# Kernel tuning notes

Hardware: AMD Instinct MI355X
Metric: run time of the kernel (lower is better)

## Reference

```python
import jax, jax.numpy as jnp
import numpy as np

# Mamba2 config (matches mamba_ssm.Mamba2 defaults used by the wrapper)
D_MODEL = 1024
D_STATE = 128
D_CONV = 4
EXPAND = 2
HEADDIM = 64
CHUNK = 256
D_INNER = EXPAND * D_MODEL            # 2048
NHEADS = D_INNER // HEADDIM           # 32
CONV_DIM = D_INNER + 2 * D_STATE      # 2304 (x, B, C share the causal conv)
D_IN_PROJ = 2 * D_INNER + 2 * D_STATE + NHEADS  # z, xBC, dt
EPS = 1e-5


def rmsnorm(x, w, eps=EPS):
    return x * jax.lax.rsqrt(jnp.mean(x * x, axis=-1, keepdims=True) + eps) * w


def setup_inputs() -> dict:
    key = jax.random.key(0)
    ks = jax.random.split(key, 8)
    B, L = 2, 2048
    def w(k, shape, sc=0.02):
        return jax.random.normal(k, shape, jnp.float32) * sc
    return {
        "x": jax.random.normal(ks[0], (B, L, D_MODEL), jnp.float32),
        "norm_w": jnp.ones((D_MODEL,), jnp.float32),
        "in_proj_w": w(ks[1], (D_IN_PROJ, D_MODEL)),
        "conv_w": w(ks[2], (CONV_DIM, 1, D_CONV), 0.2),   # depthwise kernel
        "conv_b": jnp.zeros((CONV_DIM,), jnp.float32),
        "dt_bias": w(ks[3], (NHEADS,), 1.0),
        "A_log": jnp.log(1.0 + 15.0 * jax.random.uniform(ks[4], (NHEADS,), jnp.float32)),
        "D": jnp.ones((NHEADS,), jnp.float32),
        "gnorm_w": jnp.ones((D_INNER,), jnp.float32),
        "out_proj_w": w(ks[5], (D_MODEL, D_INNER)),
    }


def _ssd(xd, a, Bm, Cm):
    """Chunked SSD scan (ssd_minimal_discrete).
    xd: (b,l,h,p) = x*dt ; a: (b,l,h) = dt*A ; Bm,Cm: (b,l,n) (ngroups=1)."""
    b, l, h, p = xd.shape
    n = Bm.shape[-1]
    nc = l // CHUNK
    xd = xd.reshape(b, nc, CHUNK, h, p)
    a = a.reshape(b, nc, CHUNK, h).transpose(0, 3, 1, 2)   # (b,h,nc,c)
    Bm = Bm.reshape(b, nc, CHUNK, n)
    Cm = Cm.reshape(b, nc, CHUNK, n)
    a_cs = jnp.cumsum(a, axis=-1)                           # (b,h,nc,c)
    # 1) intra-chunk: causal decay matrix L[t,s] = exp(sum_{s<i<=t} a_i)
    diff = a_cs[..., :, None] - a_cs[..., None, :]          # (b,h,nc,c,c)
    mask = jnp.tril(jnp.ones((CHUNK, CHUNK), bool))
    Lm = jnp.exp(jnp.where(mask, diff, 0.0)) * mask
    Y_diag = jnp.einsum("bcln,bcsn,bhcls,bcshp->bclhp", Cm, Bm, Lm, xd)
    # 2) per-chunk end states
    decay_states = jnp.exp(a_cs[..., -1:] - a_cs)           # (b,h,nc,c)
    states = jnp.einsum("bcln,bhcl,bclhp->bchpn", Bm, decay_states, xd)
    # 3) inter-chunk recurrence (vectorized segsum over the 8+1 chunk totals)
    tot = jnp.pad(a_cs[..., -1], ((0, 0), (0, 0), (1, 0)))  # (b,h,nc+1)
    tot_cs = jnp.cumsum(tot, axis=-1)
    dchunk = tot_cs[..., :, None] - tot_cs[..., None, :]    # (b,h,nc+1,nc+1)
    cmask = jnp.tril(jnp.ones((nc + 1, nc + 1), bool))
    dchunk = jnp.exp(jnp.where(cmask, dchunk, 0.0)) * cmask
    states = jnp.concatenate([jnp.zeros_like(states[:, :1]), states], axis=1)
    new_states = jnp.einsum("bhzc,bchpn->bzhpn", dchunk, states)
    init_states = new_states[:, :-1]                        # state entering each chunk
    # 4) state -> output contribution
    Y_off = jnp.einsum("bcln,bchpn,bhcl->bclhp", Cm, init_states, jnp.exp(a_cs))
    return (Y_diag + Y_off).reshape(b, l, h, p)


def reference(x, norm_w, in_proj_w, conv_w, conv_b, dt_bias, A_log, D, gnorm_w, out_proj_w):
    res = x
    u = rmsnorm(x, norm_w)
    zxbcdt = u @ in_proj_w.T                                # (b,l,d_in_proj)
    z, xBC, dt = jnp.split(zxbcdt, [D_INNER, D_INNER + CONV_DIM], axis=-1)
    # causal depthwise conv1d over (x,B,C), then SiLU
    xBC_t = jnp.pad(xBC.transpose(0, 2, 1), ((0, 0), (0, 0), (D_CONV - 1, 0)))
    conv = jax.lax.conv_general_dilated(
        xBC_t, conv_w, (1,), "VALID",
        dimension_numbers=("NCH", "OIH", "NCH"), feature_group_count=CONV_DIM)
    xBC = jax.nn.silu(conv.transpose(0, 2, 1) + conv_b)
    xs, Bm, Cm = jnp.split(xBC, [D_INNER, D_INNER + D_STATE], axis=-1)
    dt = jax.nn.softplus(dt + dt_bias)                      # (b,l,h)
    A = -jnp.exp(A_log)                                     # (h,)
    xh = xs.reshape(xs.shape[0], xs.shape[1], NHEADS, HEADDIM)
    y = _ssd(xh * dt[..., None], dt * A, Bm, Cm)
    y = y + D[None, None, :, None] * xh                     # skip term
    y = y.reshape(xs.shape)
    y = rmsnorm(y * jax.nn.silu(z), gnorm_w)                # gated RMSNorm
    return res + y @ out_proj_w.T
```

## Files before the change

### kernel.cpp

```cpp
#include <hip/hip_runtime.h>
#include <hip/hip_bf16.h>

typedef __hip_bfloat16 bf16_t;
typedef __attribute__((ext_vector_type(8))) short bfrag8;
typedef __attribute__((ext_vector_type(4))) float floatx4;

#define DM     1024
#define DI     2048
#define NHD    32
#define HD     64
#define DSTATE 128
#define CONVD  2304
#define NPROJ  4384
#define NPAD   4480
#define MR     4096
#define LL     2048
#define EPSF   1e-5f
#define PSTR   40

__device__ __forceinline__ void gl_lds16(const void* g, void* l) {
  __builtin_amdgcn_global_load_lds((const __attribute__((address_space(1))) void*)g,
                                   (__attribute__((address_space(3))) void*)l, 16, 0, 0);
}
__device__ __forceinline__ unsigned pack_bf16_rn(float a, float b) {
  unsigned ua = (__float_as_uint(a) + 0x8000u) >> 16;
  unsigned ub = (__float_as_uint(b) + 0x8000u) >> 16;
  return ua | (ub << 16);
}
__device__ __forceinline__ unsigned short bf16u(float a) {
  return (unsigned short)((__float_as_uint(a) + 0x8000u) >> 16);
}
__device__ __forceinline__ float blo(unsigned u){ return __uint_as_float(u << 16); }
__device__ __forceinline__ float bhi(unsigned u){ return __uint_as_float(u & 0xffff0000u); }

__global__ void rms1_kernel(const float* __restrict__ x, const float* __restrict__ w,
                            bf16_t* __restrict__ ub) {
  int row = blockIdx.x, t = threadIdx.x;
  float4 v = ((const float4*)(x + (long)row * DM))[t];
  float ss = v.x*v.x + v.y*v.y + v.z*v.z + v.w*v.w;
#pragma unroll
  for (int off = 32; off > 0; off >>= 1) ss += __shfl_down(ss, off, 64);
  __shared__ float red[4];
  if ((t & 63) == 0) red[t >> 6] = ss;
  __syncthreads();
  float tot = red[0] + red[1] + red[2] + red[3];
  float rs = rsqrtf(tot * (1.f / DM) + EPSF);
  float4 wv = ((const float4*)w)[t];
  bf16_t* o = ub + (long)row * DM + t * 4;
  o[0] = __float2bfloat16(v.x * rs * wv.x);
  o[1] = __float2bfloat16(v.y * rs * wv.y);
  o[2] = __float2bfloat16(v.z * rs * wv.z);
  o[3] = __float2bfloat16(v.w * rs * wv.w);
}

__global__ void cvtw1_kernel(const float* __restrict__ w, bf16_t* __restrict__ o) {
  int i4 = blockIdx.x * 256 + threadIdx.x;
  int idx = i4 * 4;
  int row = idx >> 10;
  float4 v = make_float4(0.f, 0.f, 0.f, 0.f);
  if (row < NPROJ) v = *(const float4*)(w + idx);
  bf16_t* d = o + idx;
  d[0] = __float2bfloat16(v.x); d[1] = __float2bfloat16(v.y);
  d[2] = __float2bfloat16(v.z); d[3] = __float2bfloat16(v.w);
}
__global__ void cvtw2_kernel(const float* __restrict__ w, bf16_t* __restrict__ o) {
  int i4 = blockIdx.x * 256 + threadIdx.x;
  int idx = i4 * 4;
  float4 v = *(const float4*)(w + idx);
  bf16_t* d = o + idx;
  d[0] = __float2bfloat16(v.x); d[1] = __float2bfloat16(v.y);
  d[2] = __float2bfloat16(v.z); d[3] = __float2bfloat16(v.w);
}

template<int TN, bool DO_RES, bool OUT_BF16>
__global__ __launch_bounds__(256) void gemm64_kernel(const bf16_t* __restrict__ A,
    const bf16_t* __restrict__ Bw, const float* __restrict__ resid,
    void* __restrict__ Cout, int N, int K) {
  __shared__ bf16_t As[128 * 64];
  __shared__ bf16_t Bs[TN * 64];
  const int tid = threadIdx.x;
  const int lane = tid & 63;
  const int wv = tid >> 6;
  const int l15 = lane & 15;
  const int l4 = lane >> 4;
  constexpr int MF = (TN == 128) ? 4 : 2;
  const int wm = (TN == 128) ? ((wv >> 1) << 6) : (wv << 5);
  const int wn = (TN == 128) ? ((wv & 1) << 6) : 0;
  const int tm = blockIdx.x << 7;
  const int tn = blockIdx.y * TN;

  floatx4 acc[MF][4];
#pragma unroll
  for (int i = 0; i < MF; i++)
#pragma unroll
    for (int j = 0; j < 4; j++) acc[i][j] = (floatx4){0.f, 0.f, 0.f, 0.f};

  const int r = tid >> 3;
  const int c8 = tid & 7;
  const int scol = ((c8 ^ (r & 7)) << 3);
  const bf16_t* Ag = A + (long)(tm + r) * K + scol;
  const bf16_t* Bg = Bw + (long)(tn + r) * K + scol;
  const int swz = l15 & 7;

  for (int k0 = 0; k0 < K; k0 += 64) {
#pragma unroll
    for (int q = 0; q < 4; q++)
      gl_lds16(Ag + (long)(q * 32) * K + k0, &As[q * 2048 + tid * 8]);
#pragma unroll
    for (int q = 0; q < TN / 32; q++)
      gl_lds16(Bg + (long)(q * 32) * K + k0, &Bs[q * 2048 + tid * 8]);
    __syncthreads();
#pragma unroll
    for (int kk = 0; kk < 2; kk++) {
      bfrag8 af[MF], bfr[4];
      const int ch = ((kk << 2) | l4) ^ swz;
#pragma unroll
      for (int j = 0; j < 4; j++)
        bfr[j] = *(const bfrag8*)&Bs[(wn + j * 16 + l15) * 64 + ch * 8];
#pragma unroll
      for (int i = 0; i < MF; i++)
        af[i] = *(const bfrag8*)&As[(wm + i * 16 + l15) * 64 + ch * 8];
#pragma unroll
      for (int i = 0; i < MF; i++)
#pragma unroll
        for (int j = 0; j < 4; j++)
          acc[i][j] = __builtin_amdgcn_mfma_f32_16x16x32_bf16(af[i], bfr[j], acc[i][j], 0, 0, 0);
    }
    __syncthreads();
  }
#pragma unroll
  for (int i = 0; i < MF; i++)
#pragma unroll
    for (int j = 0; j < 4; j++)
#pragma unroll
      for (int r2 = 0; r2 < 4; r2++) {
        int row = tm + wm + i * 16 + l4 * 4 + r2;
        int col = tn + wn + j * 16 + l15;
        float v = acc[i][j][r2];
        if (OUT_BF16) {
          ((bf16_t*)Cout)[(long)row * N + col] = __float2bfloat16(v);
        } else {
          if (DO_RES) v += resid[(long)row * N + col];
          ((float*)Cout)[(long)row * N + col] = v;
        }
      }
}

__global__ __launch_bounds__(256) void gemm_s_kernel(const bf16_t* __restrict__ Cmh,
                const bf16_t* __restrict__ Bmh, float* __restrict__ SL) {
  __shared__ bf16_t As[128 * 32];
  __shared__ bf16_t Bs[128 * 32];
  const int tid = threadIdx.x;
  const int lane = tid & 63;
  const int wv = tid >> 6;
  const int wm = (wv >> 1) << 6;
  const int wn = (wv & 1) << 6;
  const int bc = blockIdx.z;
  const int tm = blockIdx.x << 7;
  const int tn = blockIdx.y << 7;
  const int l15 = lane & 15;
  const int l4 = lane >> 4;
  floatx4 acc[4][4];
#pragma unroll
  for (int i = 0; i < 4; i++)
#pragma unroll
    for (int j = 0; j < 4; j++) acc[i][j] = (floatx4){0.f, 0.f, 0.f, 0.f};
  const int arow = tid >> 2;
  const int acol = (tid & 3) << 3;
  const bf16_t* Ag = Cmh + (long)bc * 256 * DSTATE + (long)(tm + arow) * DSTATE + acol;
  const bf16_t* Bg = Bmh + (long)bc * 256 * DSTATE + (long)(tn + arow) * DSTATE + acol;
  const long k64 = (long)64 * DSTATE;
  for (int k0 = 0; k0 < DSTATE; k0 += 32) {
    gl_lds16(Ag + k0, &As[tid * 8]);
    gl_lds16(Ag + k64 + k0, &As[2048 + tid * 8]);
    gl_lds16(Bg + k0, &Bs[tid * 8]);
    gl_lds16(Bg + k64 + k0, &Bs[2048 + tid * 8]);
    __syncthreads();
    bfrag8 af[4], bfr[4];
#pragma unroll
    for (int i = 0; i < 4; i++)
      af[i] = *(const bfrag8*)&As[(wm + i * 16 + l15) * 32 + l4 * 8];
#pragma unroll
    for (int j = 0; j < 4; j++)
      bfr[j] = *(const bfrag8*)&Bs[(wn + j * 16 + l15) * 32 + l4 * 8];
#pragma unroll
    for (int i = 0; i < 4; i++)
#pragma unroll
      for (int j = 0; j < 4; j++)
        acc[i][j] = __builtin_amdgcn_mfma_f32_16x16x32_bf16(af[i], bfr[j], acc[i][j], 0, 0, 0);
    __syncthreads();
  }
  float* Cb = SL + (long)bc * 65536;
#pragma unroll
  for (int i = 0; i < 4; i++)
#pragma unroll
    for (int j = 0; j < 4; j++)
#pragma unroll
      for (int r = 0; r < 4; r++)
        Cb[(long)(tm + wm + i * 16 + l4 * 4 + r) * 256 + tn + wn + j * 16 + l15] = acc[i][j][r];
}

__global__ void conv_kernel(const bf16_t* __restrict__ zxh, const float* __restrict__ cw,
                            const float* __restrict__ cb, bf16_t* __restrict__ xhb,
                            float* __restrict__ Cm,
                            bf16_t* __restrict__ Bmh, bf16_t* __restrict__ Cmh) {
  int idx = blockIdx.x * 256 + threadIdx.x;
  int c = idx % CONVD;
  int bl = idx / CONVD;
  int l = bl & (LL - 1);
  const bf16_t* base = zxh + (long)(bl - l) * NPAD + DI + c;
  float acc = cb[c];
#pragma unroll
  for (int k = 0; k < 4; k++) {
    int ls = l + k - 3;
    if (ls >= 0) acc += __bfloat162float(base[(long)ls * NPAD]) * cw[c * 4 + k];
  }
  float s = acc / (1.f + __expf(-acc));
  if (c < DI) {
    xhb[(long)bl * DI + c] = __float2bfloat16(s);
  } else if (c < DI + DSTATE) {
    Bmh[(long)bl * DSTATE + (c - DI)] = __float2bfloat16(s);
  } else {
    Cm[(long)bl * DSTATE + (c - DI - DSTATE)] = s;
    Cmh[(long)bl * DSTATE + (c - DI - DSTATE)] = __float2bfloat16(s);
  }
}

__global__ void acs_kernel(const bf16_t* __restrict__ zxh, const float* __restrict__ A_log,
                           const float* __restrict__ dtb,
                           float* __restrict__ acs, float* __restrict__ ctot,
                           float* __restrict__ dtout) {
  int blk = blockIdx.x;
  int h = blk & 31, bc = blk >> 5;
  int t = threadIdx.x, lane = t & 63, w = t >> 6;
  float Ah = -__expf(A_log[h]);
  int gl = bc * 256 + t;
  float vv = __bfloat162float(zxh[(long)gl * NPAD + (NPROJ - 32) + h]) + dtb[h];
  float sp = fmaxf(vv, 0.f) + log1pf(__expf(-fabsf(vv)));
  dtout[gl * 32 + h] = sp;
  float a = sp * Ah;
#pragma unroll
  for (int off = 1; off < 64; off <<= 1) {
    float v = __shfl_up(a, off, 64);
    if (lane >= off) a += v;
  }
  __shared__ float wsum[4];
  if (lane == 63) wsum[w] = a;
  __syncthreads();
  float base = 0.f;
  for (int i = 0; i < 4; i++) base += (i < w) ? wsum[i] : 0.f;
  a += base;
  acs[blk * 256 + t] = a;
  if (t == 255) ctot[blk] = a;
}

__global__ __launch_bounds__(256) void states2_kernel(const bf16_t* __restrict__ xhb,
    const bf16_t* __restrict__ Bmh, const float* __restrict__ dt,
    const float* __restrict__ acs, float* __restrict__ states) {
  int blk = blockIdx.x;
  int h = blk & 31, bc = blk >> 5;
  int t = threadIdx.x, lane = t & 63, wv = t >> 6;
  int l15 = lane & 15, l4 = lane >> 4;
  __shared__ unsigned short Asb[128 * 40];
  __shared__ unsigned short Bsb[64 * 40];
  float atot = acs[blk * 256 + 255];
  const int rowbase = bc * 256;
  floatx4 acc[2][4];
#pragma unroll
  for (int i = 0; i < 2; i++)
#pragma unroll
    for (int j = 0; j < 4; j++) acc[i][j] = (floatx4){0.f, 0.f, 0.f, 0.f};

  const int ls = t & 31;
  const int grp = t >> 5;
  for (int kt = 0; kt < 8; kt++) {
    __syncthreads();
    int gl = rowbase + kt * 32 + ls;
    {
      const uint4* src = (const uint4*)(Bmh + (long)gl * DSTATE + grp * 16);
      uint4 u0 = src[0], u1 = src[1];
      int n0 = grp * 16;
      Asb[(n0 + 0) * 40 + ls] = (unsigned short)(u0.x & 0xffff);
      Asb[(n0 + 1) * 40 + ls] = (unsigned short)(u0.x >> 16);
      Asb[(n0 + 2) * 40 + ls] = (unsigned short)(u0.y & 0xffff);
      Asb[(n0 + 3) * 40 + ls] = (unsigned short)(u0.y >> 16);
      Asb[(n0 + 4) * 40 + ls] = (unsigned short)(u0.z & 0xffff);
      Asb[(n0 + 5) * 40 + ls] = (unsigned short)(u0.z >> 16);
      Asb[(n0 + 6) * 40 + ls] = (unsigned short)(u0.w & 0xffff);
      Asb[(n0 + 7) * 40 + ls] = (unsigned short)(u0.w >> 16);
      Asb[(n0 + 8) * 40 + ls] = (unsigned short)(u1.x & 0xffff);
      Asb[(n0 + 9) * 40 + ls] = (unsigned short)(u1.x >> 16);
      Asb[(n0 + 10) * 40 + ls] = (unsigned short)(u1.y & 0xffff);
      Asb[(n0 + 11) * 40 + ls] = (unsigned short)(u1.y >> 16);
      Asb[(n0 + 12) * 40 + ls] = (unsigned short)(u1.z & 0xffff);
      Asb[(n0 + 13) * 40 + ls] = (unsigned short)(u1.z >> 16);
      Asb[(n0 + 14) * 40 + ls] = (unsigned short)(u1.w & 0xffff);
      Asb[(n0 + 15) * 40 + ls] = (unsigned short)(u1.w >> 16);
    }
    {
      float w = dt[gl * 32 + h] * __expf(atot - acs[blk * 256 + kt * 32 + ls]);
      uint4 u = *(const uint4*)(xhb + (long)gl * DI + h * HD + grp * 8);
      int p0 = grp * 8;
      Bsb[(p0 + 0) * 40 + ls] = bf16u(blo(u.x) * w);
      Bsb[(p0 + 1) * 40 + ls] = bf16u(bhi(u.x) * w);
      Bsb[(p0 + 2) * 40 + ls] = bf16u(blo(u.y) * w);
      Bsb[(p0 + 3) * 40 + ls] = bf16u(bhi(u.y) * w);
      Bsb[(p0 + 4) * 40 + ls] = bf16u(blo(u.z) * w);
      Bsb[(p0 + 5) * 40 + ls] = bf16u(bhi(u.z) * w);
      Bsb[(p0 + 6) * 40 + ls] = bf16u(blo(u.w) * w);
      Bsb[(p0 + 7) * 40 + ls] = bf16u(bhi(u.w) * w);
    }
    __syncthreads();
    bfrag8 af[2], bfr[4];
#pragma unroll
    for (int i = 0; i < 2; i++)
      af[i] = *(const bfrag8*)&Asb[(wv * 32 + i * 16 + l15) * 40 + l4 * 8];
#pragma unroll
    for (int j = 0; j < 4; j++)
      bfr[j] = *(const bfrag8*)&Bsb[(j * 16 + l15) * 40 + l4 * 8];
#pragma unroll
    for (int i = 0; i < 2; i++)
#pragma unroll
      for (int j = 0; j < 4; j++)
        acc[i][j] = __builtin_amdgcn_mfma_f32_16x16x32_bf16(af[i], bfr[j], acc[i][j], 0, 0, 0);
  }
#pragma unroll
  for (int i = 0; i < 2; i++)
#pragma unroll
    for (int j = 0; j < 4; j++) {
      int n_base = wv * 32 + i * 16 + l4 * 4;
      int p = j * 16 + l15;
      *(float4*)&states[(long)blk * 8192 + p * 128 + n_base] =
          make_float4(acc[i][j][0], acc[i][j][1], acc[i][j][2], acc[i][j][3]);
    }
}

__global__ void scan_kernel(const float* __restrict__ states, const float* __restrict__ ctot,
                            bf16_t* __restrict__ initsb) {
  int id = blockIdx.x * 256 + threadIdx.x;
  int pn = id & 8191;
  int bh = id >> 13;
  int b = bh >> 5, h = bh & 31;
  float S = 0.f;
#pragma unroll
  for (int c = 0; c < 8; c++) {
    int blk = (b * 8 + c) * 32 + h;
    initsb[(long)blk * 8192 + pn] = __float2bfloat16(S);
    S = __expf(ctot[blk]) * S + states[(long)blk * 8192 + pn];
  }
}

__global__ __launch_bounds__(256, 4) void yk2_kernel(const float* __restrict__ SL,
     const float* __restrict__ Cmp, const bf16_t* __restrict__ xhb,
     const bf16_t* __restrict__ zxh, const float* __restrict__ dt,
     const float* __restrict__ acs, const bf16_t* __restrict__ initsb,
     const float* __restrict__ Dp, bf16_t* __restrict__ yg, float* __restrict__ ssqp) {
  int bi = blockIdx.x;
  int mh = bi & 1, h = (bi >> 1) & 31, bc = bi >> 6;
  int ablk = bc * 32 + h;
  int t = threadIdx.x;
  int lane = t & 63, wv = t >> 6;
  int l15 = lane & 15, l4 = lane >> 4;
  __shared__ float acsS[256];
  __shared__ __align__(16) char ubuf[128 * 66 * 4];
  bf16_t* Ps = (bf16_t*)ubuf;
  bf16_t* Xs = (bf16_t*)(ubuf + 128 * PSTR * 2);
  float* Yt = (float*)ubuf;

  acsS[t] = acs[ablk * 256 + t];
  __syncthreads();
  const int l_loc = t >> 1, half = t & 1;
  const int l = mh * 128 + l_loc;
  const float al = acsS[l];
  const float eAl = __expf(al);
  const int rowbase = bc * 256;
  const float* SLb = SL + (long)bc * 65536 + (long)l * 256;

  floatx4 acc[2][4];
#pragma unroll
  for (int i = 0; i < 2; i++)
#pragma unroll
    for (int j = 0; j < 4; j++) acc[i][j] = (floatx4){0.f, 0.f, 0.f, 0.f};

  const int nkd = (mh + 1) * 4;
  for (int kt = 0; kt < nkd + 4; kt++) {
    __syncthreads();
    if (kt < nkd) {
      int s0 = kt * 32 + half * 16;
      unsigned pk[8];
      const float4* Sg = (const float4*)(SLb + s0);
#pragma unroll
      for (int q = 0; q < 4; q++) {
        float4 v = Sg[q];
        int sb = s0 + q * 4;
        float p0 = (sb + 0 <= l) ? v.x * __expf(al - acsS[sb + 0]) : 0.f;
        float p1 = (sb + 1 <= l) ? v.y * __expf(al - acsS[sb + 1]) : 0.f;
        float p2 = (sb + 2 <= l) ? v.z * __expf(al - acsS[sb + 2]) : 0.f;
        float p3 = (sb + 3 <= l) ? v.w * __expf(al - acsS[sb + 3]) : 0.f;
        pk[q * 2 + 0] = pack_bf16_rn(p0, p1);
        pk[q * 2 + 1] = pack_bf16_rn(p2, p3);
      }
      uint4* pw = (uint4*)&Ps[l_loc * PSTR + half * 16];
      pw[0] = make_uint4(pk[0], pk[1], pk[2], pk[3]);
      pw[1] = make_uint4(pk[4], pk[5], pk[6], pk[7]);
      int p4 = t & 15, sh = t >> 4;
#pragma unroll
      for (int r = 0; r < 2; r++) {
        int s = sh + r * 16;
        int gl = rowbase + kt * 32 + s;
        float w = dt[gl * 32 + h];
        uint2 u = *(const uint2*)(xhb + (long)gl * DI + h * HD + p4 * 4);
        Xs[(p4 * 4 + 0) * PSTR + s] = __float2bfloat16(blo(u.x) * w);
        Xs[(p4 * 4 + 1) * PSTR + s] = __float2bfloat16(bhi(u.x) * w);
        Xs[(p4 * 4 + 2) * PSTR + s] = __float2bfloat16(blo(u.y) * w);
        Xs[(p4 * 4 + 3) * PSTR + s] = __float2bfloat16(bhi(u.y) * w);
      }
    } else {
      int n0 = (kt - nkd) * 32;
      unsigned pk[8];
      const float4* Cg = (const float4*)(Cmp + (long)(rowbase + l) * DSTATE + n0 + half * 16);
#pragma unroll
      for (int q = 0; q < 4; q++) {
        float4 v = Cg[q];
        pk[q * 2 + 0] = pack_bf16_rn(v.x * eAl, v.y * eAl);
        pk[q * 2 + 1] = pack_bf16_rn(v.z * eAl, v.w * eAl);
      }
      uint4* pw = (uint4*)&Ps[l_loc * PSTR + half * 16];
      pw[0] = make_uint4(pk[0], pk[1], pk[2], pk[3]);
      pw[1] = make_uint4(pk[4], pk[5], pk[6], pk[7]);
      int p_loc = t >> 2, quad = t & 3;
      uint4 u = *(const uint4*)(initsb + (long)ablk * 8192 + p_loc * 128 + n0 + quad * 8);
      *(uint4*)&Xs[p_loc * PSTR + quad * 8] = u;
    }
    __syncthreads();
    bfrag8 bfr[4];
#pragma unroll
    for (int j = 0; j < 4; j++)
      bfr[j] = *(const bfrag8*)&Xs[(j * 16 + l15) * PSTR + l4 * 8];
#pragma unroll
    for (int i = 0; i < 2; i++) {
      bfrag8 af = *(const bfrag8*)&Ps[(wv * 32 + i * 16 + l15) * PSTR + l4 * 8];
#pragma unroll
      for (int j = 0; j < 4; j++)
        acc[i][j] = __builtin_amdgcn_mfma_f32_16x16x32_bf16(af, bfr[j], acc[i][j], 0, 0, 0);
    }
  }
  __syncthreads();
#pragma unroll
  for (int i = 0; i < 2; i++)
#pragma unroll
    for (int j = 0; j < 4; j++)
#pragma unroll
      for (int r = 0; r < 4; r++)
        Yt[(wv * 32 + i * 16 + l4 * 4 + r) * 66 + j * 16 + l15] = acc[i][j][r];
  __syncthreads();
  {
    int row_l = t >> 1;
    int ch = (t & 1) * 32;
    long rowg = rowbase + mh * 128 + row_l;
    float Dh = Dp[h];
    float ss = 0.f;
#pragma unroll
    for (int it = 0; it < 4; it++) {
      int c = ch + it * 8;
      float4 y0 = *(const float4*)&Yt[row_l * 66 + c];
      float4 y1 = *(const float4*)&Yt[row_l * 66 + c + 4];
      uint4 ux = *(const uint4*)(xhb + rowg * DI + h * HD + c);
      uint4 uz = *(const uint4*)(zxh + rowg * NPAD + h * HD + c);
      float xv[8] = {blo(ux.x), bhi(ux.x), blo(ux.y), bhi(ux.y),
                     blo(ux.z), bhi(ux.z), blo(ux.w), bhi(ux.w)};
      float zv[8] = {blo(uz.x), bhi(uz.x), blo(uz.y), bhi(uz.y),
                     blo(uz.z), bhi(uz.z), blo(uz.w), bhi(uz.w)};
      float yv[8] = {y0.x, y0.y, y0.z, y0.w, y1.x, y1.y, y1.z, y1.w};
      unsigned o[4];
#pragma unroll
      for (int q = 0; q < 4; q++) {
        float v0 = (yv[q * 2 + 0] + Dh * xv[q * 2 + 0]) *
                   (zv[q * 2 + 0] / (1.f + __expf(-zv[q * 2 + 0])));
        float v1 = (yv[q * 2 + 1] + Dh * xv[q * 2 + 1]) *
                   (zv[q * 2 + 1] / (1.f + __expf(-zv[q * 2 + 1])));
        ss += v0 * v0 + v1 * v1;
        o[q] = pack_bf16_rn(v0, v1);
      }
      *(uint4*)(yg + rowg * DI + h * HD + c) = make_uint4(o[0], o[1], o[2], o[3]);
    }
    ss += __shfl_xor(ss, 1, 64);
    if ((t & 1) == 0) ssqp[rowg * 32 + h] = ss;
  }
}

__global__ void gnorm2_kernel(const bf16_t* __restrict__ yg, const float* __restrict__ ssqp,
                              const float* __restrict__ gw, bf16_t* __restrict__ yn) {
  int row = blockIdx.x, t = threadIdx.x;
  __shared__ float rsS;
  if (t < 64) {
    float v = (t < 32) ? ssqp[row * 32 + t] : 0.f;
#pragma unroll
    for (int off = 16; off > 0; off >>= 1) v += __shfl_down(v, off, 64);
    if (t == 0) rsS = rsqrtf(v * (1.f / DI) + EPSF);
  }
  __syncthreads();
  float rs = rsS;
  uint4 u = *(const uint4*)(yg + (long)row * DI + t * 8);
  float4 g0 = ((const float4*)gw)[t * 2];
  float4 g1 = ((const float4*)gw)[t * 2 + 1];
  unsigned o0 = pack_bf16_rn(blo(u.x) * rs * g0.x, bhi(u.x) * rs * g0.y);
  unsigned o1 = pack_bf16_rn(blo(u.y) * rs * g0.z, bhi(u.y) * rs * g0.w);
  unsigned o2 = pack_bf16_rn(blo(u.z) * rs * g1.x, bhi(u.z) * rs * g1.y);
  unsigned o3 = pack_bf16_rn(blo(u.w) * rs * g1.z, bhi(u.w) * rs * g1.w);
  *(uint4*)(yn + (long)row * DI + t * 8) = make_uint4(o0, o1, o2, o3);
}

extern "C" void kernel_launch(void* const* d_in, const int* in_sizes, int n_in,
                              void* d_out, int out_size, void* d_ws, size_t ws_size,
                              hipStream_t stream) {
  const float* x    = (const float*)d_in[0];
  const float* nw   = (const float*)d_in[1];
  const float* w1   = (const float*)d_in[2];
  const float* cw   = (const float*)d_in[3];
  const float* cb   = (const float*)d_in[4];
  const float* dtb  = (const float*)d_in[5];
  const float* alog = (const float*)d_in[6];
  const float* Dp   = (const float*)d_in[7];
  const float* gw   = (const float*)d_in[8];
  const float* w2   = (const float*)d_in[9];
  float* out = (float*)d_out;

  char* ws = (char*)d_ws;
  size_t off = 0;
  auto alloc = [&](size_t bytes) -> void* {
    void* p = ws + off;
    off += (bytes + 255) & ~(size_t)255;
    return p;
  };
  bf16_t* ub     = (bf16_t*)alloc((size_t)MR * DM * 2);
  bf16_t* w1b    = (bf16_t*)alloc((size_t)NPAD * DM * 2);
  bf16_t* w2b    = (bf16_t*)alloc((size_t)DM * DI * 2);
  bf16_t* zxh    = (bf16_t*)alloc((size_t)MR * NPAD * 2);
  bf16_t* xhb    = (bf16_t*)alloc((size_t)MR * DI * 2);
  float* Cm      = (float*)alloc((size_t)MR * DSTATE * 4);
  bf16_t* Bmh    = (bf16_t*)alloc((size_t)MR * DSTATE * 2);
  bf16_t* Cmh    = (bf16_t*)alloc((size_t)MR * DSTATE * 2);
  float* SL      = (float*)alloc((size_t)16 * 256 * 256 * 4);
  float* dt      = (float*)alloc((size_t)MR * NHD * 4);
  float* acs     = (float*)alloc((size_t)512 * 256 * 4);
  float* ctot    = (float*)alloc((size_t)512 * 4);
  float* states  = (float*)alloc((size_t)512 * 8192 * 4);
  bf16_t* initsb = (bf16_t*)alloc((size_t)512 * 8192 * 2);
  bf16_t* yg     = (bf16_t*)alloc((size_t)MR * DI * 2);
  float* ssqp    = (float*)alloc((size_t)MR * NHD * 4);
  bf16_t* yn     = (bf16_t*)alloc((size_t)MR * DI * 2);
  if (off > ws_size) return;

  rms1_kernel<<<MR, 256, 0, stream>>>(x, nw, ub);
  cvtw1_kernel<<<(NPAD * DM / 4) / 256, 256, 0, stream>>>(w1, w1b);
  cvtw2_kernel<<<(DM * DI / 4) / 256, 256, 0, stream>>>(w2, w2b);
  gemm64_kernel<128, false, true><<<dim3(MR / 128, NPAD / 128), 256, 0, stream>>>(
      ub, w1b, nullptr, zxh, NPAD, DM);
  conv_kernel<<<(MR * CONVD) / 256, 256, 0, stream>>>(zxh, cw, cb, xhb, Cm, Bmh, Cmh);
  acs_kernel<<<512, 256, 0, stream>>>(zxh, alog, dtb, acs, ctot, dt);
  gemm_s_kernel<<<dim3(2, 2, 16), 256, 0, stream>>>(Cmh, Bmh, SL);
  states2_kernel<<<512, 256, 0, stream>>>(xhb, Bmh, dt, acs, states);
  scan_kernel<<<(2 * 32 * 8192) / 256, 256, 0, stream>>>(states, ctot, initsb);
  yk2_kernel<<<1024, 256, 0, stream>>>(SL, Cm, xhb, zxh, dt, acs, initsb, Dp, yg, ssqp);
  gnorm2_kernel<<<MR, 256, 0, stream>>>(yg, ssqp, gw, yn);
  gemm64_kernel<64, true, false><<<dim3(MR / 128, DM / 64), 256, 0, stream>>>(
      yn, w2b, x, out, DM, DI);
}
```

Before: 306.4 us.

## Vectorize conv, pre-transpose x*dt and B, bf16 states, merge weight casts

Merges the two weight-conversion kernels into one launch. Rewrites the depthwise conv so each thread handles 8 channels over 4 timesteps with vector loads and stores, and drops the fp32 C copy. Adds a kernel that writes x*dt, decay-weighted x*dt and B into transposed bf16 buffers, so the states and output kernels read MFMA fragments straight from global memory instead of transposing through LDS. Chunk states are now stored in bf16, which halves their traffic but adds rounding to the scan inputs.

Measured after the change: 296.8 us. -3.1%, faster.

```diff
diff --git a/kernel.cpp b/kernel.cpp
--- a/kernel.cpp
+++ b/kernel.cpp
@@ -32,6 +32,10 @@
 }
 __device__ __forceinline__ float blo(unsigned u){ return __uint_as_float(u << 16); }
 __device__ __forceinline__ float bhi(unsigned u){ return __uint_as_float(u & 0xffff0000u); }
+__device__ __forceinline__ void unp8(uint4 u, float* v) {
+  v[0]=blo(u.x); v[1]=bhi(u.x); v[2]=blo(u.y); v[3]=bhi(u.y);
+  v[4]=blo(u.z); v[5]=bhi(u.z); v[6]=blo(u.w); v[7]=bhi(u.w);
+}
 
 __global__ void rms1_kernel(const float* __restrict__ x, const float* __restrict__ w,
                             bf16_t* __restrict__ ub) {
@@ -53,23 +57,26 @@
   o[3] = __float2bfloat16(v.w * rs * wv.w);
 }
 
-__global__ void cvtw1_kernel(const float* __restrict__ w, bf16_t* __restrict__ o) {
+#define W1CNT (NPAD * DM / 4)
+#define W2CNT (DM * DI / 4)
+__global__ void cvtw_kernel(const float* __restrict__ w1, const float* __restrict__ w2,
+                            bf16_t* __restrict__ o1, bf16_t* __restrict__ o2) {
   int i4 = blockIdx.x * 256 + threadIdx.x;
-  int idx = i4 * 4;
-  int row = idx >> 10;
-  float4 v = make_float4(0.f, 0.f, 0.f, 0.f);
-  if (row < NPROJ) v = *(const float4*)(w + idx);
-  bf16_t* d = o + idx;
-  d[0] = __float2bfloat16(v.x); d[1] = __float2bfloat16(v.y);
-  d[2] = __float2bfloat16(v.z); d[3] = __float2bfloat16(v.w);
-}
-__global__ void cvtw2_kernel(const float* __restrict__ w, bf16_t* __restrict__ o) {
-  int i4 = blockIdx.x * 256 + threadIdx.x;
-  int idx = i4 * 4;
-  float4 v = *(const float4*)(w + idx);
-  bf16_t* d = o + idx;
-  d[0] = __float2bfloat16(v.x); d[1] = __float2bfloat16(v.y);
-  d[2] = __float2bfloat16(v.z); d[3] = __float2bfloat16(v.w);
+  if (i4 < W1CNT) {
+    int idx = i4 * 4;
+    int row = idx >> 10;
+    float4 v = make_float4(0.f, 0.f, 0.f, 0.f);
+    if (row < NPROJ) v = *(const float4*)(w1 + idx);
+    bf16_t* d = o1 + idx;
+    d[0] = __float2bfloat16(v.x); d[1] = __float2bfloat16(v.y);
+    d[2] = __float2bfloat16(v.z); d[3] = __float2bfloat16(v.w);
+  } else {
+    int idx = (i4 - W1CNT) * 4;
+    float4 v = *(const float4*)(w2 + idx);
+    bf16_t* d = o2 + idx;
+    d[0] = __float2bfloat16(v.x); d[1] = __float2bfloat16(v.y);
+    d[2] = __float2bfloat16(v.z); d[3] = __float2bfloat16(v.w);
+  }
 }
 
 template<int TN, bool DO_RES, bool OUT_BF16>
@@ -200,29 +207,54 @@
         Cb[(long)(tm + wm + i * 16 + l4 * 4 + r) * 256 + tn + wn + j * 16 + l15] = acc[i][j][r];
 }
 
-__global__ void conv_kernel(const bf16_t* __restrict__ zxh, const float* __restrict__ cw,
-                            const float* __restrict__ cb, bf16_t* __restrict__ xhb,
-                            float* __restrict__ Cm,
-                            bf16_t* __restrict__ Bmh, bf16_t* __restrict__ Cmh) {
-  int idx = blockIdx.x * 256 + threadIdx.x;
-  int c = idx % CONVD;
-  int bl = idx / CONVD;
-  int l = bl & (LL - 1);
-  const bf16_t* base = zxh + (long)(bl - l) * NPAD + DI + c;
-  float acc = cb[c];
-#pragma unroll
-  for (int k = 0; k < 4; k++) {
-    int ls = l + k - 3;
-    if (ls >= 0) acc += __bfloat162float(base[(long)ls * NPAD]) * cw[c * 4 + k];
-  }
-  float s = acc / (1.f + __expf(-acc));
-  if (c < DI) {
-    xhb[(long)bl * DI + c] = __float2bfloat16(s);
-  } else if (c < DI + DSTATE) {
-    Bmh[(long)bl * DSTATE + (c - DI)] = __float2bfloat16(s);
-  } else {
-    Cm[(long)bl * DSTATE + (c - DI - DSTATE)] = s;
-    Cmh[(long)bl * DSTATE + (c - DI - DSTATE)] = __float2bfloat16(s);
+__global__ __launch_bounds__(256) void conv4_kernel(const bf16_t* __restrict__ zxh,
+    const float* __restrict__ cw, const float* __restrict__ cb,
+    bf16_t* __restrict__ xhb, bf16_t* __restrict__ Bmh, bf16_t* __restrict__ Cmh) {
+  int g = blockIdx.x * 256 + threadIdx.x;
+  int cg = g % 288;
+  int blt = g / 288;
+  int c0 = cg * 8;
+  long bl0 = (long)blt * 4;
+  int l0 = (int)(bl0 & (LL - 1));
+  const bf16_t* base = zxh + bl0 * NPAD + DI + c0;
+  float rv[7][8];
+#pragma unroll
+  for (int j = 0; j < 7; j++) {
+    int dj = j - 3;
+    if (l0 + dj >= 0) {
+      uint4 u = *(const uint4*)(base + (long)dj * NPAD);
+      unp8(u, rv[j]);
+    } else {
+#pragma unroll
+      for (int q = 0; q < 8; q++) rv[j][q] = 0.f;
+    }
+  }
+  float4 wq[8];
+#pragma unroll
+  for (int q = 0; q < 8; q++) wq[q] = ((const float4*)cw)[c0 + q];
+  float bias[8];
+  *(float4*)&bias[0] = *(const float4*)(cb + c0);
+  *(float4*)&bias[4] = *(const float4*)(cb + c0 + 4);
+#pragma unroll
+  for (int i = 0; i < 4; i++) {
+    unsigned o[4];
+#pragma unroll
+    for (int q2 = 0; q2 < 4; q2++) {
+      float rr[2];
+#pragma unroll
+      for (int e = 0; e < 2; e++) {
+        int q = q2 * 2 + e;
+        float a = bias[q] + wq[q].x * rv[i][q] + wq[q].y * rv[i + 1][q]
+                + wq[q].z * rv[i + 2][q] + wq[q].w * rv[i + 3][q];
+        rr[e] = a / (1.f + __expf(-a));
+      }
+      o[q2] = pack_bf16_rn(rr[0], rr[1]);
+    }
+    uint4 ov = make_uint4(o[0], o[1], o[2], o[3]);
+    long bl = bl0 + i;
+    if (c0 < DI)               *(uint4*)(xhb + bl * DI + c0) = ov;
+    else if (c0 < DI + DSTATE) *(uint4*)(Bmh + bl * DSTATE + (c0 - DI)) = ov;
+    else                       *(uint4*)(Cmh + bl * DSTATE + (c0 - DI - DSTATE)) = ov;
   }
 }
 
@@ -254,70 +286,87 @@
   if (t == 255) ctot[blk] = a;
 }
 
-__global__ __launch_bounds__(256) void states2_kernel(const bf16_t* __restrict__ xhb,
+__global__ __launch_bounds__(256) void xdt_kernel(const bf16_t* __restrict__ xhb,
     const bf16_t* __restrict__ Bmh, const float* __restrict__ dt,
-    const float* __restrict__ acs, float* __restrict__ states) {
+    const float* __restrict__ acs, bf16_t* __restrict__ xdT,
+    bf16_t* __restrict__ xdTe, bf16_t* __restrict__ BmT) {
+  __shared__ unsigned short Tb[9216];
   int blk = blockIdx.x;
-  int h = blk & 31, bc = blk >> 5;
+  int t = threadIdx.x;
+  if (blk < 512) {
+    unsigned short* T1 = Tb;
+    unsigned short* T2 = Tb + 4608;
+    int h = blk & 31, bc = blk >> 5;
+    float atot = acs[blk * 256 + 255];
+    int l_loc = t >> 2, pg = t & 3;
+    for (int lt = 0; lt < 4; lt++) {
+      int gl = bc * 256 + lt * 64 + l_loc;
+      float w1 = dt[gl * 32 + h];
+      float w2 = w1 * __expf(atot - acs[blk * 256 + lt * 64 + l_loc]);
+      const uint4* src = (const uint4*)(xhb + (long)gl * DI + h * HD + pg * 16);
+      uint4 u0 = src[0], u1 = src[1];
+      float v[16];
+      unp8(u0, v); unp8(u1, v + 8);
+      __syncthreads();
+#pragma unroll
+      for (int q = 0; q < 16; q++) {
+        T1[(pg * 16 + q) * 72 + l_loc] = bf16u(v[q] * w1);
+        T2[(pg * 16 + q) * 72 + l_loc] = bf16u(v[q] * w2);
+      }
+      __syncthreads();
+      long orow = ((long)blk * 64 + l_loc) * 256 + lt * 64 + pg * 16;
+      *(uint4*)(xdT + orow)      = *(uint4*)&T1[l_loc * 72 + pg * 16];
+      *(uint4*)(xdT + orow + 8)  = *(uint4*)&T1[l_loc * 72 + pg * 16 + 8];
+      *(uint4*)(xdTe + orow)     = *(uint4*)&T2[l_loc * 72 + pg * 16];
+      *(uint4*)(xdTe + orow + 8) = *(uint4*)&T2[l_loc * 72 + pg * 16 + 8];
+    }
+  } else {
+    unsigned short* T = Tb;
+    int bc = blk - 512;
+    int l_loc = t >> 2, ng = t & 3;
+    for (int lt = 0; lt < 4; lt++) {
+      int gl = bc * 256 + lt * 64 + l_loc;
+      const uint4* src = (const uint4*)(Bmh + (long)gl * DSTATE + ng * 32);
+      uint4 u[4];
+#pragma unroll
+      for (int q = 0; q < 4; q++) u[q] = src[q];
+      __syncthreads();
+      const unsigned short* us = (const unsigned short*)u;
+#pragma unroll
+      for (int e = 0; e < 32; e++)
+        T[(ng * 32 + e) * 72 + l_loc] = us[e];
+      __syncthreads();
+      int n = t >> 1, lg2 = t & 1;
+      long orow = ((long)bc * 128 + n) * 256 + lt * 64 + lg2 * 32;
+#pragma unroll
+      for (int q = 0; q < 4; q++)
+        *(uint4*)(BmT + orow + q * 8) = *(uint4*)&T[n * 72 + lg2 * 32 + q * 8];
+    }
+  }
+}
+
+__global__ __launch_bounds__(256) void states3_kernel(const bf16_t* __restrict__ xdTe,
+    const bf16_t* __restrict__ BmT, bf16_t* __restrict__ states) {
+  int blk = blockIdx.x;
+  int bc = blk >> 5;
   int t = threadIdx.x, lane = t & 63, wv = t >> 6;
   int l15 = lane & 15, l4 = lane >> 4;
-  __shared__ unsigned short Asb[128 * 40];
-  __shared__ unsigned short Bsb[64 * 40];
-  float atot = acs[blk * 256 + 255];
-  const int rowbase = bc * 256;
   floatx4 acc[2][4];
 #pragma unroll
   for (int i = 0; i < 2; i++)
 #pragma unroll
     for (int j = 0; j < 4; j++) acc[i][j] = (floatx4){0.f, 0.f, 0.f, 0.f};
-
-  const int ls = t & 31;
-  const int grp = t >> 5;
+  const bf16_t* arow = BmT + (long)bc * 128 * 256;
+  const bf16_t* brow = xdTe + (long)blk * 64 * 256;
+#pragma unroll
   for (int kt = 0; kt < 8; kt++) {
-    __syncthreads();
-    int gl = rowbase + kt * 32 + ls;
-    {
-      const uint4* src = (const uint4*)(Bmh + (long)gl * DSTATE + grp * 16);
-      uint4 u0 = src[0], u1 = src[1];
-      int n0 = grp * 16;
-      Asb[(n0 + 0) * 40 + ls] = (unsigned short)(u0.x & 0xffff);
-      Asb[(n0 + 1) * 40 + ls] = (unsigned short)(u0.x >> 16);
-      Asb[(n0 + 2) * 40 + ls] = (unsigned short)(u0.y & 0xffff);
-      Asb[(n0 + 3) * 40 + ls] = (unsigned short)(u0.y >> 16);
-      Asb[(n0 + 4) * 40 + ls] = (unsigned short)(u0.z & 0xffff);
-      Asb[(n0 + 5) * 40 + ls] = (unsigned short)(u0.z >> 16);
-      Asb[(n0 + 6) * 40 + ls] = (unsigned short)(u0.w & 0xffff);
-      Asb[(n0 + 7) * 40 + ls] = (unsigned short)(u0.w >> 16);
-      Asb[(n0 + 8) * 40 + ls] = (unsigned short)(u1.x & 0xffff);
-      Asb[(n0 + 9) * 40 + ls] = (unsigned short)(u1.x >> 16);
-      Asb[(n0 + 10) * 40 + ls] = (unsigned short)(u1.y & 0xffff);
-      Asb[(n0 + 11) * 40 + ls] = (unsigned short)(u1.y >> 16);
-      Asb[(n0 + 12) * 40 + ls] = (unsigned short)(u1.z & 0xffff);
-      Asb[(n0 + 13) * 40 + ls] = (unsigned short)(u1.z >> 16);
-      Asb[(n0 + 14) * 40 + ls] = (unsigned short)(u1.w & 0xffff);
-      Asb[(n0 + 15) * 40 + ls] = (unsigned short)(u1.w >> 16);
-    }
-    {
-      float w = dt[gl * 32 + h] * __expf(atot - acs[blk * 256 + kt * 32 + ls]);
-      uint4 u = *(const uint4*)(xhb + (long)gl * DI + h * HD + grp * 8);
-      int p0 = grp * 8;
-      Bsb[(p0 + 0) * 40 + ls] = bf16u(blo(u.x) * w);
-      Bsb[(p0 + 1) * 40 + ls] = bf16u(bhi(u.x) * w);
-      Bsb[(p0 + 2) * 40 + ls] = bf16u(blo(u.y) * w);
-      Bsb[(p0 + 3) * 40 + ls] = bf16u(bhi(u.y) * w);
-      Bsb[(p0 + 4) * 40 + ls] = bf16u(blo(u.z) * w);
-      Bsb[(p0 + 5) * 40 + ls] = bf16u(bhi(u.z) * w);
-      Bsb[(p0 + 6) * 40 + ls] = bf16u(blo(u.w) * w);
-      Bsb[(p0 + 7) * 40 + ls] = bf16u(bhi(u.w) * w);
-    }
-    __syncthreads();
     bfrag8 af[2], bfr[4];
 #pragma unroll
     for (int i = 0; i < 2; i++)
-      af[i] = *(const bfrag8*)&Asb[(wv * 32 + i * 16 + l15) * 40 + l4 * 8];
+      af[i] = *(const bfrag8*)(arow + (long)(wv * 32 + i * 16 + l15) * 256 + kt * 32 + l4 * 8);
 #pragma unroll
     for (int j = 0; j < 4; j++)
-      bfr[j] = *(const bfrag8*)&Bsb[(j * 16 + l15) * 40 + l4 * 8];
+      bfr[j] = *(const bfrag8*)(brow + (long)(j * 16 + l15) * 256 + kt * 32 + l4 * 8);
 #pragma unroll
     for (int i = 0; i < 2; i++)
 #pragma unroll
@@ -330,12 +379,13 @@
     for (int j = 0; j < 4; j++) {
       int n_base = wv * 32 + i * 16 + l4 * 4;
       int p = j * 16 + l15;
-      *(float4*)&states[(long)blk * 8192 + p * 128 + n_base] =
-          make_float4(acc[i][j][0], acc[i][j][1], acc[i][j][2], acc[i][j][3]);
-    }
-}
-
-__global__ void scan_kernel(const float* __restrict__ states, const float* __restrict__ ctot,
+      unsigned lo = pack_bf16_rn(acc[i][j][0], acc[i][j][1]);
+      unsigned hi = pack_bf16_rn(acc[i][j][2], acc[i][j][3]);
+      *(uint2*)(states + (long)blk * 8192 + p * 128 + n_base) = make_uint2(lo, hi);
+    }
+}
+
+__global__ void scan_kernel(const bf16_t* __restrict__ states, const float* __restrict__ ctot,
                             bf16_t* __restrict__ initsb) {
   int id = blockIdx.x * 256 + threadIdx.x;
   int pn = id & 8191;
@@ -346,14 +396,14 @@
   for (int c = 0; c < 8; c++) {
     int blk = (b * 8 + c) * 32 + h;
     initsb[(long)blk * 8192 + pn] = __float2bfloat16(S);
-    S = __expf(ctot[blk]) * S + states[(long)blk * 8192 + pn];
+    S = __expf(ctot[blk]) * S + __bfloat162float(states[(long)blk * 8192 + pn]);
   }
 }
 
 __global__ __launch_bounds__(256, 4) void yk2_kernel(const float* __restrict__ SL,
-     const float* __restrict__ Cmp, const bf16_t* __restrict__ xhb,
-     const bf16_t* __restrict__ zxh, const float* __restrict__ dt,
-     const float* __restrict__ acs, const bf16_t* __restrict__ initsb,
+     const bf16_t* __restrict__ Cmh, const bf16_t* __restrict__ xhb,
+     const bf16_t* __restrict__ zxh, const float* __restrict__ acs,
+     const bf16_t* __restrict__ initsb, const bf16_t* __restrict__ xdT,
      const float* __restrict__ Dp, bf16_t* __restrict__ yg, float* __restrict__ ssqp) {
   int bi = blockIdx.x;
   int mh = bi & 1, h = (bi >> 1) & 31, bc = bi >> 6;
@@ -364,7 +414,6 @@
   __shared__ float acsS[256];
   __shared__ __align__(16) char ubuf[128 * 66 * 4];
   bf16_t* Ps = (bf16_t*)ubuf;
-  bf16_t* Xs = (bf16_t*)(ubuf + 128 * PSTR * 2);
   float* Yt = (float*)ubuf;
 
   acsS[t] = acs[ablk * 256 + t];
@@ -375,6 +424,7 @@
   const float eAl = __expf(al);
   const int rowbase = bc * 256;
   const float* SLb = SL + (long)bc * 65536 + (long)l * 256;
+  const bf16_t* xrow = xdT + (long)ablk * 64 * 256;
 
   floatx4 acc[2][4];
 #pragma unroll
@@ -403,40 +453,32 @@
       uint4* pw = (uint4*)&Ps[l_loc * PSTR + half * 16];
       pw[0] = make_uint4(pk[0], pk[1], pk[2], pk[3]);
       pw[1] = make_uint4(pk[4], pk[5], pk[6], pk[7]);
-      int p4 = t & 15, sh = t >> 4;
-#pragma unroll
-      for (int r = 0; r < 2; r++) {
-        int s = sh + r * 16;
-        int gl = rowbase + kt * 32 + s;
-        float w = dt[gl * 32 + h];
-        uint2 u = *(const uint2*)(xhb + (long)gl * DI + h * HD + p4 * 4);
-        Xs[(p4 * 4 + 0) * PSTR + s] = __float2bfloat16(blo(u.x) * w);
-        Xs[(p4 * 4 + 1) * PSTR + s] = __float2bfloat16(bhi(u.x) * w);
-        Xs[(p4 * 4 + 2) * PSTR + s] = __float2bfloat16(blo(u.y) * w);
-        Xs[(p4 * 4 + 3) * PSTR + s] = __float2bfloat16(bhi(u.y) * w);
-      }
     } else {
       int n0 = (kt - nkd) * 32;
       unsigned pk[8];
-      const float4* Cg = (const float4*)(Cmp + (long)(rowbase + l) * DSTATE + n0 + half * 16);
-#pragma unroll
-      for (int q = 0; q < 4; q++) {
-        float4 v = Cg[q];
-        pk[q * 2 + 0] = pack_bf16_rn(v.x * eAl, v.y * eAl);
-        pk[q * 2 + 1] = pack_bf16_rn(v.z * eAl, v.w * eAl);
-      }
+      const uint4* Cg = (const uint4*)(Cmh + (long)(rowbase + l) * DSTATE + n0 + half * 16);
+      uint4 u0 = Cg[0], u1 = Cg[1];
+      float cv[16];
+      unp8(u0, cv); unp8(u1, cv + 8);
+#pragma unroll
+      for (int q = 0; q < 8; q++)
+        pk[q] = pack_bf16_rn(cv[q * 2] * eAl, cv[q * 2 + 1] * eAl);
       uint4* pw = (uint4*)&Ps[l_loc * PSTR + half * 16];
       pw[0] = make_uint4(pk[0], pk[1], pk[2], pk[3]);
       pw[1] = make_uint4(pk[4], pk[5], pk[6], pk[7]);
-      int p_loc = t >> 2, quad = t & 3;
-      uint4 u = *(const uint4*)(initsb + (long)ablk * 8192 + p_loc * 128 + n0 + quad * 8);
-      *(uint4*)&Xs[p_loc * PSTR + quad * 8] = u;
     }
     __syncthreads();
     bfrag8 bfr[4];
-#pragma unroll
-    for (int j = 0; j < 4; j++)
-      bfr[j] = *(const bfrag8*)&Xs[(j * 16 + l15) * PSTR + l4 * 8];
+    if (kt < nkd) {
+#pragma unroll
+      for (int j = 0; j < 4; j++)
+        bfr[j] = *(const bfrag8*)(xrow + (long)(j * 16 + l15) * 256 + kt * 32 + l4 * 8);
+    } else {
+      int n0 = (kt - nkd) * 32;
+#pragma unroll
+      for (int j = 0; j < 4; j++)
+        bfr[j] = *(const bfrag8*)(initsb + (long)ablk * 8192 + (j * 16 + l15) * 128 + n0 + l4 * 8);
+    }
 #pragma unroll
     for (int i = 0; i < 2; i++) {
       bfrag8 af = *(const bfrag8*)&Ps[(wv * 32 + i * 16 + l15) * PSTR + l4 * 8];
@@ -467,10 +509,8 @@
       float4 y1 = *(const float4*)&Yt[row_l * 66 + c + 4];
       uint4 ux = *(const uint4*)(xhb + rowg * DI + h * HD + c);
       uint4 uz = *(const uint4*)(zxh + rowg * NPAD + h * HD + c);
-      float xv[8] = {blo(ux.x), bhi(ux.x), blo(ux.y), bhi(ux.y),
-                     blo(ux.z), bhi(ux.z), blo(ux.w), bhi(ux.w)};
-      float zv[8] = {blo(uz.x), bhi(uz.x), blo(uz.y), bhi(uz.y),
-                     blo(uz.z), bhi(uz.z), blo(uz.w), bhi(uz.w)};
+      float xv[8], zv[8];
+      unp8(ux, xv); unp8(uz, zv);
       float yv[8] = {y0.x, y0.y, y0.z, y0.w, y1.x, y1.y, y1.z, y1.w};
       unsigned o[4];
 #pragma unroll
@@ -538,31 +578,33 @@
   bf16_t* w2b    = (bf16_t*)alloc((size_t)DM * DI * 2);
   bf16_t* zxh    = (bf16_t*)alloc((size_t)MR * NPAD * 2);
   bf16_t* xhb    = (bf16_t*)alloc((size_t)MR * DI * 2);
-  float* Cm      = (float*)alloc((size_t)MR * DSTATE * 4);
   bf16_t* Bmh    = (bf16_t*)alloc((size_t)MR * DSTATE * 2);
   bf16_t* Cmh    = (bf16_t*)alloc((size_t)MR * DSTATE * 2);
   float* SL      = (float*)alloc((size_t)16 * 256 * 256 * 4);
   float* dt      = (float*)alloc((size_t)MR * NHD * 4);
   float* acs     = (float*)alloc((size_t)512 * 256 * 4);
   float* ctot    = (float*)alloc((size_t)512 * 4);
-  float* states  = (float*)alloc((size_t)512 * 8192 * 4);
+  bf16_t* states = (bf16_t*)alloc((size_t)512 * 8192 * 2);
   bf16_t* initsb = (bf16_t*)alloc((size_t)512 * 8192 * 2);
+  bf16_t* xdT    = (bf16_t*)alloc((size_t)512 * 64 * 256 * 2);
+  bf16_t* xdTe   = (bf16_t*)alloc((size_t)512 * 64 * 256 * 2);
+  bf16_t* BmT    = (bf16_t*)alloc((size_t)16 * 128 * 256 * 2);
   bf16_t* yg     = (bf16_t*)alloc((size_t)MR * DI * 2);
   float* ssqp    = (float*)alloc((size_t)MR * NHD * 4);
   bf16_t* yn     = (bf16_t*)alloc((size_t)MR * DI * 2);
   if (off > ws_size) return;
 
   rms1_kernel<<<MR, 256, 0, stream>>>(x, nw, ub);
-  cvtw1_kernel<<<(NPAD * DM / 4) / 256, 256, 0, stream>>>(w1, w1b);
-  cvtw2_kernel<<<(DM * DI / 4) / 256, 256, 0, stream>>>(w2, w2b);
+  cvtw_kernel<<<(W1CNT + W2CNT) / 256, 256, 0, stream>>>(w1, w2, w1b, w2b);
   gemm64_kernel<128, false, true><<<dim3(MR / 128, NPAD / 128), 256, 0, stream>>>(
       ub, w1b, nullptr, zxh, NPAD, DM);
-  conv_kernel<<<(MR * CONVD) / 256, 256, 0, stream>>>(zxh, cw, cb, xhb, Cm, Bmh, Cmh);
+  conv4_kernel<<<(1024 * 288) / 256, 256, 0, stream>>>(zxh, cw, cb, xhb, Bmh, Cmh);
   acs_kernel<<<512, 256, 0, stream>>>(zxh, alog, dtb, acs, ctot, dt);
+  xdt_kernel<<<528, 256, 0, stream>>>(xhb, Bmh, dt, acs, xdT, xdTe, BmT);
   gemm_s_kernel<<<dim3(2, 2, 16), 256, 0, stream>>>(Cmh, Bmh, SL);
-  states2_kernel<<<512, 256, 0, stream>>>(xhb, Bmh, dt, acs, states);
+  states3_kernel<<<512, 256, 0, stream>>>(xdTe, BmT, states);
   scan_kernel<<<(2 * 32 * 8192) / 256, 256, 0, stream>>>(states, ctot, initsb);
-  yk2_kernel<<<1024, 256, 0, stream>>>(SL, Cm, xhb, zxh, dt, acs, initsb, Dp, yg, ssqp);
+  yk2_kernel<<<1024, 256, 0, stream>>>(SL, Cmh, xhb, zxh, acs, initsb, xdT, Dp, yg, ssqp);
   gnorm2_kernel<<<MR, 256, 0, stream>>>(yg, ssqp, gw, yn);
   gemm64_kernel<64, true, false><<<dim3(MR / 128, DM / 64), 256, 0, stream>>>(
       yn, w2b, x, out, DM, DI);
```
